# Optimization experiments

Measured on AMD Instinct MI355X. Metric: run time of the kernel, lower is better.

The kernel has to match this reference:

```python
import jax, jax.numpy as jnp
import numpy as np

B, T, C, HS = 4, 2048, 1024, 64

def setup_inputs() -> dict:
    key = jax.random.key(0)
    k1, k2, k3, k4 = jax.random.split(key, 4)
    x = jax.random.normal(k1, (B, T, C), dtype=jnp.float32)
    # torch Linear default init scale ~ 1/sqrt(fan_in); scale weights similarly
    s = C ** -0.5
    Wq = jax.random.normal(k2, (C, HS), dtype=jnp.float32) * s
    Wk = jax.random.normal(k3, (C, HS), dtype=jnp.float32) * s
    Wv = jax.random.normal(k4, (C, HS), dtype=jnp.float32) * s
    return {"x": x, "Wq": Wq, "Wk": Wk, "Wv": Wv}

def reference(x, Wq, Wk, Wv):
    B_, T_, C_ = x.shape
    q = x @ Wq          # [B,T,HS]
    k = x @ Wk          # [B,T,HS]
    v = x @ Wv          # [B,T,HS]
    scale = C_ ** -0.5  # note: module scales by input dim C, not head_size
    w = jnp.einsum('bqh,bkh->bqk', q, k) * scale  # [B,T,T]
    causal = jnp.tril(jnp.ones((T_, T_), dtype=bool))
    w = jnp.where(causal, w, -jnp.inf)
    a = jax.nn.softmax(w, axis=-1)  # dropout is identity (eval / drop_rate=0)
    return jnp.einsum('bqk,bkh->bqh', a, v)
```

## Files before the change

kernel.cpp:

```cpp
#include <hip/hip_runtime.h>
#include <math.h>

#define B_  4
#define T_  2048
#define C_  1024
#define HS_ 64
#define M_  (B_*T_)
#define NCAT 192
#define SCALE_ 0.03125f

typedef unsigned short ushort_t;
typedef short bf16x8 __attribute__((ext_vector_type(8)));
typedef float f32x4 __attribute__((ext_vector_type(4)));

static __device__ __forceinline__ unsigned short f2bf(float f) {
    union { float f; unsigned int u; } c; c.f = f;
    unsigned int u = c.u;
    return (unsigned short)((u + 0x7FFFu + ((u >> 16) & 1u)) >> 16);
}
static __device__ __forceinline__ unsigned short f2bf_fast(float f) {
    union { float f; unsigned int u; } c; c.f = f;
    return (unsigned short)((c.u + 0x8000u) >> 16);
}

__global__ void wconv_kernel(const float* __restrict__ Wq, const float* __restrict__ Wk,
                             const float* __restrict__ Wv, ushort_t* __restrict__ wt) {
    int idx = (blockIdx.x * 256 + threadIdx.x) * 4;
    int n = idx >> 10;
    int k0 = idx & 1023;
    const float* W = (n < 64) ? Wq : (n < 128) ? Wk : Wv;
    int nn = n & 63;
    ushort_t o0 = f2bf(W[(k0 + 0) * HS_ + nn]);
    ushort_t o1 = f2bf(W[(k0 + 1) * HS_ + nn]);
    ushort_t o2 = f2bf(W[(k0 + 2) * HS_ + nn]);
    ushort_t o3 = f2bf(W[(k0 + 3) * HS_ + nn]);
    uint2 d;
    d.x = (unsigned)o0 | ((unsigned)o1 << 16);
    d.y = (unsigned)o2 | ((unsigned)o3 << 16);
    *(uint2*)(wt + (size_t)n * C_ + k0) = d;
}

__global__ __launch_bounds__(512, 4) void proj_kernel(const float* __restrict__ x,
    const ushort_t* __restrict__ wt,
    ushort_t* __restrict__ qws, ushort_t* __restrict__ kws, ushort_t* __restrict__ vt) {
    __shared__ __align__(16) f32x4 red[4][12 * 64];

    int tid  = threadIdx.x;
    int wid  = tid >> 6;
    int lane = tid & 63;
    int qd   = lane >> 4;
    int lq   = lane & 15;
    int r0   = blockIdx.x * 16;

    f32x4 acc[12];
    #pragma unroll
    for (int i = 0; i < 12; i++) acc[i] = (f32x4){0.f,0.f,0.f,0.f};

    const float*    xp = x  + (size_t)(r0 + lq) * C_ + wid * 128 + qd * 8;
    const ushort_t* wp = wt + (size_t)lq * C_ + wid * 128 + qd * 8;

    #pragma unroll
    for (int i = 0; i < 4; i++) {
        float4 a0 = *(const float4*)(xp + i * 32);
        float4 a1 = *(const float4*)(xp + i * 32 + 4);
        union { bf16x8 v; ushort_t u[8]; } af;
        af.u[0] = f2bf(a0.x); af.u[1] = f2bf(a0.y); af.u[2] = f2bf(a0.z); af.u[3] = f2bf(a0.w);
        af.u[4] = f2bf(a1.x); af.u[5] = f2bf(a1.y); af.u[6] = f2bf(a1.z); af.u[7] = f2bf(a1.w);
        #pragma unroll
        for (int nt = 0; nt < 12; nt++) {
            bf16x8 bv = *(const bf16x8*)(wp + (size_t)nt * 16 * C_ + i * 32);
            acc[nt] = __builtin_amdgcn_mfma_f32_16x16x32_bf16(af.v, bv, acc[nt], 0, 0, 0);
        }
    }

    if (wid >= 4) {
        #pragma unroll
        for (int nt = 0; nt < 12; nt++) red[wid - 4][nt * 64 + lane] = acc[nt];
    }
    __syncthreads();
    if (wid < 4) {
        #pragma unroll
        for (int nt = 0; nt < 12; nt++) acc[nt] += red[wid][nt * 64 + lane];
    }
    __syncthreads();
    if (wid == 2 || wid == 3) {
        #pragma unroll
        for (int nt = 0; nt < 12; nt++) red[wid][nt * 64 + lane] = acc[nt];
    }
    __syncthreads();
    if (wid < 2) {
        #pragma unroll
        for (int nt = 0; nt < 12; nt++) acc[nt] += red[wid + 2][nt * 64 + lane];
    }
    __syncthreads();
    if (wid == 1) {
        #pragma unroll
        for (int nt = 0; nt < 12; nt++) red[0][nt * 64 + lane] = acc[nt];
    }
    __syncthreads();
    if (wid == 0) {
        #pragma unroll
        for (int nt = 0; nt < 12; nt++) {
            acc[nt] += red[0][nt * 64 + lane];
            int outn = nt >> 2;
            int col  = (nt & 3) * 16 + lq;
            #pragma unroll
            for (int r = 0; r < 4; r++) {
                int row = r0 + qd * 4 + r;
                float v = acc[nt][r];
                if (outn == 0) v *= SCALE_;
                ushort_t val = f2bf(v);
                if (outn == 0)      qws[(size_t)row * HS_ + col] = val;
                else if (outn == 1) kws[(size_t)row * HS_ + col] = val;
                else {
                    int b = row >> 11, t = row & 2047;
                    vt[((size_t)b * 64 + col) * T_ + t] = val;
                }
            }
        }
    }
}

__global__ __launch_bounds__(512, 2) void flash_kernel(const ushort_t* __restrict__ qws,
    const ushort_t* __restrict__ kws, const ushort_t* __restrict__ vt,
    float* __restrict__ out) {
    __shared__ __align__(16) unsigned char pool[18432];

    int tid  = threadIdx.x;
    int wid  = tid >> 6;
    int lane = tid & 63;
    int qd   = lane >> 4;
    int lq   = lane & 15;
    int ts   = wid >> 2;
    int ws   = wid & 3;

    int batch = blockIdx.y;
    int p     = blockIdx.x;
    int tile  = ts ? (127 - p) : p;
    int q0    = tile * 16;
    int qrow  = q0 + lq;
    int grow  = batch * T_ + qrow;
    int nU    = (tile + 4) >> 2;

    bf16x8 qf[2];
    #pragma unroll
    for (int st = 0; st < 2; st++)
        qf[st] = *(const bf16x8*)(qws + (size_t)grow * HS_ + st * 32 + qd * 8);

    float lsum = 0.f;
    f32x4 O[4];
    #pragma unroll
    for (int nt = 0; nt < 4; nt++) O[nt] = (f32x4){0.f,0.f,0.f,0.f};

    ushort_t* pw = (ushort_t*)pool + wid * 1152 + lq * 72;
    const ushort_t* kp    = kws + (size_t)batch * T_ * HS_;
    const ushort_t* vbase = vt  + (size_t)batch * 64 * T_;

    for (int u = ws; u < nU; u += 4) {
        int kb = u * 64;

        bf16x8 kf[8], vf[8];
        #pragma unroll
        for (int sub = 0; sub < 4; sub++)
            #pragma unroll
            for (int st = 0; st < 2; st++)
                kf[sub * 2 + st] = *(const bf16x8*)(kp + (size_t)(kb + sub * 16 + lq) * HS_ + st * 32 + qd * 8);
        #pragma unroll
        for (int nt = 0; nt < 4; nt++)
            #pragma unroll
            for (int kk = 0; kk < 2; kk++)
                vf[nt * 2 + kk] = *(const bf16x8*)(vbase + ((size_t)nt * 16 + lq) * T_ + kb + kk * 32 + qd * 8);

        f32x4 S[4];
        #pragma unroll
        for (int sub = 0; sub < 4; sub++) {
            f32x4 s = (f32x4){0.f,0.f,0.f,0.f};
            #pragma unroll
            for (int st = 0; st < 2; st++)
                s = __builtin_amdgcn_mfma_f32_16x16x32_bf16(kf[sub * 2 + st], qf[st], s, 0, 0, 0);
            S[sub] = s;
        }

        if (kb + 64 > q0) {
            #pragma unroll
            for (int sub = 0; sub < 4; sub++)
                #pragma unroll
                for (int r = 0; r < 4; r++) {
                    int key = kb + sub * 16 + qd * 4 + r;
                    float pv = (key <= qrow) ? __expf(S[sub][r]) : 0.f;
                    S[sub][r] = pv;
                    lsum += pv;
                }
        } else {
            #pragma unroll
            for (int sub = 0; sub < 4; sub++)
                #pragma unroll
                for (int r = 0; r < 4; r++) {
                    float pv = __expf(S[sub][r]);
                    S[sub][r] = pv;
                    lsum += pv;
                }
        }

        #pragma unroll
        for (int sub = 0; sub < 4; sub++) {
            uint2 d;
            d.x = (unsigned)f2bf_fast(S[sub][0]) | ((unsigned)f2bf_fast(S[sub][1]) << 16);
            d.y = (unsigned)f2bf_fast(S[sub][2]) | ((unsigned)f2bf_fast(S[sub][3]) << 16);
            *(uint2*)(pw + sub * 16 + qd * 4) = d;
        }
        bf16x8 pf0 = *(const bf16x8*)(pw + qd * 8);
        bf16x8 pf1 = *(const bf16x8*)(pw + 32 + qd * 8);

        #pragma unroll
        for (int nt = 0; nt < 4; nt++) {
            O[nt] = __builtin_amdgcn_mfma_f32_16x16x32_bf16(vf[nt * 2 + 0], pf0, O[nt], 0, 0, 0);
            O[nt] = __builtin_amdgcn_mfma_f32_16x16x32_bf16(vf[nt * 2 + 1], pf1, O[nt], 0, 0, 0);
        }
    }

    f32x4* red  = (f32x4*)pool;
    float* lred = (float*)(pool + 16384);
    __syncthreads();
    if (ws >= 2) {
        int sl = ts * 2 + (ws - 2);
        f32x4* rs = red + (size_t)sl * 256;
        #pragma unroll
        for (int nt = 0; nt < 4; nt++) rs[nt * 64 + lane] = O[nt];
        lred[sl * 64 + lane] = lsum;
    }
    __syncthreads();
    if (ws < 2) {
        int sl = ts * 2 + ws;
        f32x4* rs = red + (size_t)sl * 256;
        #pragma unroll
        for (int nt = 0; nt < 4; nt++) O[nt] += rs[nt * 64 + lane];
        lsum += lred[sl * 64 + lane];
    }
    __syncthreads();
    if (ws == 1) {
        int sl = ts * 2;
        f32x4* rs = red + (size_t)sl * 256;
        #pragma unroll
        for (int nt = 0; nt < 4; nt++) rs[nt * 64 + lane] = O[nt];
        lred[sl * 64 + lane] = lsum;
    }
    __syncthreads();
    if (ws == 0) {
        int sl = ts * 2;
        f32x4* rs = red + (size_t)sl * 256;
        #pragma unroll
        for (int nt = 0; nt < 4; nt++) O[nt] += rs[nt * 64 + lane];
        lsum += lred[sl * 64 + lane];
        lsum += __shfl_xor(lsum, 16, 64);
        lsum += __shfl_xor(lsum, 32, 64);
        float li = 1.f / lsum;
        #pragma unroll
        for (int nt = 0; nt < 4; nt++) {
            f32x4 o = O[nt] * li;
            *(f32x4*)(out + (size_t)grow * HS_ + nt * 16 + qd * 4) = o;
        }
    }
}

extern "C" void kernel_launch(void* const* d_in, const int* in_sizes, int n_in,
                              void* d_out, int out_size, void* d_ws, size_t ws_size,
                              hipStream_t stream) {
    const float* x  = (const float*)d_in[0];
    const float* Wq = (const float*)d_in[1];
    const float* Wk = (const float*)d_in[2];
    const float* Wv = (const float*)d_in[3];
    float* out = (float*)d_out;

    ushort_t* wt  = (ushort_t*)d_ws;
    ushort_t* qws = wt  + (size_t)NCAT * C_;
    ushort_t* kws = qws + (size_t)M_ * HS_;
    ushort_t* vt  = kws + (size_t)M_ * HS_;

    wconv_kernel<<<NCAT * C_ / (256 * 4), 256, 0, stream>>>(Wq, Wk, Wv, wt);
    proj_kernel<<<512, 512, 0, stream>>>(x, wt, qws, kws, vt);
    flash_kernel<<<dim3(64, 4), 512, 0, stream>>>(qws, kws, vt, out);
}
```

Baseline: 121.3 us.

## Restructure QKV projection into LDS-tiled GEMM with 2D warp tiling

The projection kernel used to split K across 8 warps, with each warp reading its own bf16 weights and fp32 x straight from global memory, then reduce across warps through shared memory. It now stages 32-row x tiles (converted to bf16) and the full 192-column weight slice into padded LDS per 128-wide K step, and assigns each warp a 16x48 output tile. This removes the cross-warp reduction and the redundant global weight loads, at the cost of two barriers per K step, fewer blocks (256) and a lower occupancy bound.

```diff
diff --git a/kernel.cpp b/kernel.cpp
--- a/kernel.cpp
+++ b/kernel.cpp
@@ -40,82 +40,85 @@
     *(uint2*)(wt + (size_t)n * C_ + k0) = d;
 }
 
-__global__ __launch_bounds__(512, 4) void proj_kernel(const float* __restrict__ x,
+__global__ __launch_bounds__(512, 2) void proj_kernel(const float* __restrict__ x,
     const ushort_t* __restrict__ wt,
     ushort_t* __restrict__ qws, ushort_t* __restrict__ kws, ushort_t* __restrict__ vt) {
-    __shared__ __align__(16) f32x4 red[4][12 * 64];
+    __shared__ __align__(16) ushort_t lds[32 * 136 + 192 * 136];
+    ushort_t* xs  = lds;
+    ushort_t* wsl = lds + 32 * 136;
 
     int tid  = threadIdx.x;
     int wid  = tid >> 6;
     int lane = tid & 63;
     int qd   = lane >> 4;
     int lq   = lane & 15;
-    int r0   = blockIdx.x * 16;
-
-    f32x4 acc[12];
-    #pragma unroll
-    for (int i = 0; i < 12; i++) acc[i] = (f32x4){0.f,0.f,0.f,0.f};
-
-    const float*    xp = x  + (size_t)(r0 + lq) * C_ + wid * 128 + qd * 8;
-    const ushort_t* wp = wt + (size_t)lq * C_ + wid * 128 + qd * 8;
-
-    #pragma unroll
-    for (int i = 0; i < 4; i++) {
-        float4 a0 = *(const float4*)(xp + i * 32);
-        float4 a1 = *(const float4*)(xp + i * 32 + 4);
-        union { bf16x8 v; ushort_t u[8]; } af;
-        af.u[0] = f2bf(a0.x); af.u[1] = f2bf(a0.y); af.u[2] = f2bf(a0.z); af.u[3] = f2bf(a0.w);
-        af.u[4] = f2bf(a1.x); af.u[5] = f2bf(a1.y); af.u[6] = f2bf(a1.z); af.u[7] = f2bf(a1.w);
-        #pragma unroll
-        for (int nt = 0; nt < 12; nt++) {
-            bf16x8 bv = *(const bf16x8*)(wp + (size_t)nt * 16 * C_ + i * 32);
-            acc[nt] = __builtin_amdgcn_mfma_f32_16x16x32_bf16(af.v, bv, acc[nt], 0, 0, 0);
-        }
-    }
-
-    if (wid >= 4) {
-        #pragma unroll
-        for (int nt = 0; nt < 12; nt++) red[wid - 4][nt * 64 + lane] = acc[nt];
-    }
-    __syncthreads();
-    if (wid < 4) {
-        #pragma unroll
-        for (int nt = 0; nt < 12; nt++) acc[nt] += red[wid][nt * 64 + lane];
-    }
-    __syncthreads();
-    if (wid == 2 || wid == 3) {
-        #pragma unroll
-        for (int nt = 0; nt < 12; nt++) red[wid][nt * 64 + lane] = acc[nt];
-    }
-    __syncthreads();
-    if (wid < 2) {
-        #pragma unroll
-        for (int nt = 0; nt < 12; nt++) acc[nt] += red[wid + 2][nt * 64 + lane];
-    }
-    __syncthreads();
-    if (wid == 1) {
-        #pragma unroll
-        for (int nt = 0; nt < 12; nt++) red[0][nt * 64 + lane] = acc[nt];
-    }
-    __syncthreads();
-    if (wid == 0) {
-        #pragma unroll
-        for (int nt = 0; nt < 12; nt++) {
-            acc[nt] += red[0][nt * 64 + lane];
-            int outn = nt >> 2;
-            int col  = (nt & 3) * 16 + lq;
-            #pragma unroll
-            for (int r = 0; r < 4; r++) {
-                int row = r0 + qd * 4 + r;
-                float v = acc[nt][r];
-                if (outn == 0) v *= SCALE_;
-                ushort_t val = f2bf(v);
-                if (outn == 0)      qws[(size_t)row * HS_ + col] = val;
-                else if (outn == 1) kws[(size_t)row * HS_ + col] = val;
-                else {
-                    int b = row >> 11, t = row & 2047;
-                    vt[((size_t)b * 64 + col) * T_ + t] = val;
-                }
+    int mi   = wid >> 2;
+    int nj   = wid & 3;
+    int r0   = blockIdx.x * 32;
+
+    f32x4 acc[3];
+    #pragma unroll
+    for (int i = 0; i < 3; i++) acc[i] = (f32x4){0.f,0.f,0.f,0.f};
+
+    int xrow0 = tid >> 5,  xc0 = (tid & 31);
+    int xrow1 = (tid + 512) >> 5, xc1 = ((tid + 512) & 31);
+
+    for (int ks = 0; ks < 8; ks++) {
+        float4 xv0 = *(const float4*)(x + (size_t)(r0 + xrow0) * C_ + ks * 128 + xc0 * 4);
+        float4 xv1 = *(const float4*)(x + (size_t)(r0 + xrow1) * C_ + ks * 128 + xc1 * 4);
+        uint4 wv[6];
+        #pragma unroll
+        for (int j = 0; j < 6; j++) {
+            int cid = tid + j * 512;
+            int n   = cid >> 4, c16 = cid & 15;
+            wv[j] = *(const uint4*)(wt + (size_t)n * C_ + ks * 128 + c16 * 8);
+        }
+        __syncthreads();
+        {
+            uint2 p0, p1;
+            p0.x = (unsigned)f2bf(xv0.x) | ((unsigned)f2bf(xv0.y) << 16);
+            p0.y = (unsigned)f2bf(xv0.z) | ((unsigned)f2bf(xv0.w) << 16);
+            p1.x = (unsigned)f2bf(xv1.x) | ((unsigned)f2bf(xv1.y) << 16);
+            p1.y = (unsigned)f2bf(xv1.z) | ((unsigned)f2bf(xv1.w) << 16);
+            *(uint2*)(xs + xrow0 * 136 + xc0 * 4) = p0;
+            *(uint2*)(xs + xrow1 * 136 + xc1 * 4) = p1;
+            #pragma unroll
+            for (int j = 0; j < 6; j++) {
+                int cid = tid + j * 512;
+                int n   = cid >> 4, c16 = cid & 15;
+                *(uint4*)(wsl + n * 136 + c16 * 8) = wv[j];
+            }
+        }
+        __syncthreads();
+
+        const ushort_t* xrow = xs + (mi * 16 + lq) * 136;
+        #pragma unroll
+        for (int i = 0; i < 4; i++) {
+            bf16x8 af = *(const bf16x8*)(xrow + qd * 8 + i * 32);
+            #pragma unroll
+            for (int nt = 0; nt < 3; nt++) {
+                bf16x8 bv = *(const bf16x8*)(wsl + (nj * 48 + nt * 16 + lq) * 136 + qd * 8 + i * 32);
+                acc[nt] = __builtin_amdgcn_mfma_f32_16x16x32_bf16(af, bv, acc[nt], 0, 0, 0);
+            }
+        }
+    }
+
+    #pragma unroll
+    for (int nt = 0; nt < 3; nt++) {
+        int n    = nj * 48 + nt * 16 + lq;
+        int outn = n >> 6;
+        int col  = n & 63;
+        #pragma unroll
+        for (int r = 0; r < 4; r++) {
+            int row = r0 + mi * 16 + qd * 4 + r;
+            float v = acc[nt][r];
+            if (outn == 0) v *= SCALE_;
+            ushort_t val = f2bf(v);
+            if (outn == 0)      qws[(size_t)row * HS_ + col] = val;
+            else if (outn == 1) kws[(size_t)row * HS_ + col] = val;
+            else {
+                int b = row >> 11, t = row & 2047;
+                vt[((size_t)b * 64 + col) * T_ + t] = val;
             }
         }
     }
@@ -278,6 +281,6 @@
     ushort_t* vt  = kws + (size_t)M_ * HS_;
 
     wconv_kernel<<<NCAT * C_ / (256 * 4), 256, 0, stream>>>(Wq, Wk, Wv, wt);
-    proj_kernel<<<512, 512, 0, stream>>>(x, wt, qws, kws, vt);
+    proj_kernel<<<256, 512, 0, stream>>>(x, wt, qws, kws, vt);
     flash_kernel<<<dim3(64, 4), 512, 0, stream>>>(qws, kws, vt, out);
 }
```

New measurement: 134.2 us. +10.6%, slower.

## Pre-pack weights in MFMA fragment order and stage bf16 x tile in LDS

Applied to the files above, without the earlier changes.

The weight conversion kernel now writes bf16 weights already laid out in per-lane MFMA fragment order, so each lane in the projection kernel reads one contiguous 16-byte chunk instead of strided rows. The projection kernel loads its 16-row x tile with coalesced float4 reads, converts it to bf16 once into padded shared memory, and then feeds MFMA from LDS. The shared pool is reused for the cross-wave reduction, which adds an extra barrier and needs 48KB of LDS per block, and that may limit occupancy.

```diff
diff --git a/kernel.cpp b/kernel.cpp
--- a/kernel.cpp
+++ b/kernel.cpp
@@ -8,6 +8,7 @@
 #define M_  (B_*T_)
 #define NCAT 192
 #define SCALE_ 0.03125f
+#define XPAD 1032
 
 typedef unsigned short ushort_t;
 typedef short bf16x8 __attribute__((ext_vector_type(8)));
@@ -24,26 +25,25 @@
 }
 
 __global__ void wconv_kernel(const float* __restrict__ Wq, const float* __restrict__ Wk,
-                             const float* __restrict__ Wv, ushort_t* __restrict__ wt) {
-    int idx = (blockIdx.x * 256 + threadIdx.x) * 4;
-    int n = idx >> 10;
-    int k0 = idx & 1023;
-    const float* W = (n < 64) ? Wq : (n < 128) ? Wk : Wv;
-    int nn = n & 63;
-    ushort_t o0 = f2bf(W[(k0 + 0) * HS_ + nn]);
-    ushort_t o1 = f2bf(W[(k0 + 1) * HS_ + nn]);
-    ushort_t o2 = f2bf(W[(k0 + 2) * HS_ + nn]);
-    ushort_t o3 = f2bf(W[(k0 + 3) * HS_ + nn]);
-    uint2 d;
-    d.x = (unsigned)o0 | ((unsigned)o1 << 16);
-    d.y = (unsigned)o2 | ((unsigned)o3 << 16);
-    *(uint2*)(wt + (size_t)n * C_ + k0) = d;
+                             const float* __restrict__ Wv, ushort_t* __restrict__ wtp) {
+    int l = threadIdx.x & 63;
+    int g = blockIdx.x * 4 + (threadIdx.x >> 6);
+    int c  = g / 12;
+    int nt = g % 12;
+    const float* W = (nt < 4) ? Wq : (nt < 8) ? Wk : Wv;
+    int nn = (nt & 3) * 16 + (l & 15);
+    int k0 = c * 32 + (l >> 4) * 8;
+    union { bf16x8 v; ushort_t u[8]; } pk;
+    #pragma unroll
+    for (int e = 0; e < 8; e++)
+        pk.u[e] = f2bf(W[(size_t)(k0 + e) * HS_ + nn]);
+    *(bf16x8*)(wtp + ((size_t)g * 64 + l) * 8) = pk.v;
 }
 
 __global__ __launch_bounds__(512, 4) void proj_kernel(const float* __restrict__ x,
-    const ushort_t* __restrict__ wt,
+    const ushort_t* __restrict__ wtp,
     ushort_t* __restrict__ qws, ushort_t* __restrict__ kws, ushort_t* __restrict__ vt) {
-    __shared__ __align__(16) f32x4 red[4][12 * 64];
+    __shared__ __align__(16) unsigned char pool[49152];
 
     int tid  = threadIdx.x;
     int wid  = tid >> 6;
@@ -52,27 +52,47 @@
     int lq   = lane & 15;
     int r0   = blockIdx.x * 16;
 
+    ushort_t* xs = (ushort_t*)pool;
+    {
+        float4 xv[8];
+        #pragma unroll
+        for (int j = 0; j < 8; j++) {
+            int flat4 = j * 512 + tid;
+            int row   = flat4 >> 8;
+            int c4    = flat4 & 255;
+            xv[j] = *(const float4*)(x + (size_t)(r0 + row) * C_ + c4 * 4);
+        }
+        #pragma unroll
+        for (int j = 0; j < 8; j++) {
+            int flat4 = j * 512 + tid;
+            int row   = flat4 >> 8;
+            int c4    = flat4 & 255;
+            uint2 p;
+            p.x = (unsigned)f2bf(xv[j].x) | ((unsigned)f2bf(xv[j].y) << 16);
+            p.y = (unsigned)f2bf(xv[j].z) | ((unsigned)f2bf(xv[j].w) << 16);
+            *(uint2*)(xs + row * XPAD + c4 * 4) = p;
+        }
+    }
+    __syncthreads();
+
     f32x4 acc[12];
     #pragma unroll
     for (int i = 0; i < 12; i++) acc[i] = (f32x4){0.f,0.f,0.f,0.f};
 
-    const float*    xp = x  + (size_t)(r0 + lq) * C_ + wid * 128 + qd * 8;
-    const ushort_t* wp = wt + (size_t)lq * C_ + wid * 128 + qd * 8;
-
+    const ushort_t* xrow = xs + lq * XPAD + wid * 128 + qd * 8;
     #pragma unroll
     for (int i = 0; i < 4; i++) {
-        float4 a0 = *(const float4*)(xp + i * 32);
-        float4 a1 = *(const float4*)(xp + i * 32 + 4);
-        union { bf16x8 v; ushort_t u[8]; } af;
-        af.u[0] = f2bf(a0.x); af.u[1] = f2bf(a0.y); af.u[2] = f2bf(a0.z); af.u[3] = f2bf(a0.w);
-        af.u[4] = f2bf(a1.x); af.u[5] = f2bf(a1.y); af.u[6] = f2bf(a1.z); af.u[7] = f2bf(a1.w);
+        bf16x8 af = *(const bf16x8*)(xrow + i * 32);
         #pragma unroll
         for (int nt = 0; nt < 12; nt++) {
-            bf16x8 bv = *(const bf16x8*)(wp + (size_t)nt * 16 * C_ + i * 32);
-            acc[nt] = __builtin_amdgcn_mfma_f32_16x16x32_bf16(af.v, bv, acc[nt], 0, 0, 0);
-        }
-    }
-
+            bf16x8 bv = *(const bf16x8*)(wtp +
+                (((size_t)(wid * 4 + i) * 12 + nt) * 64 + lane) * 8);
+            acc[nt] = __builtin_amdgcn_mfma_f32_16x16x32_bf16(af, bv, acc[nt], 0, 0, 0);
+        }
+    }
+
+    __syncthreads();
+    f32x4 (*red)[12 * 64] = (f32x4 (*)[12 * 64])pool;
     if (wid >= 4) {
         #pragma unroll
         for (int nt = 0; nt < 12; nt++) red[wid - 4][nt * 64 + lane] = acc[nt];
@@ -272,12 +292,12 @@
     const float* Wv = (const float*)d_in[3];
     float* out = (float*)d_out;
 
-    ushort_t* wt  = (ushort_t*)d_ws;
-    ushort_t* qws = wt  + (size_t)NCAT * C_;
+    ushort_t* wtp = (ushort_t*)d_ws;
+    ushort_t* qws = wtp + (size_t)384 * 64 * 8;
     ushort_t* kws = qws + (size_t)M_ * HS_;
     ushort_t* vt  = kws + (size_t)M_ * HS_;
 
-    wconv_kernel<<<NCAT * C_ / (256 * 4), 256, 0, stream>>>(Wq, Wk, Wv, wt);
-    proj_kernel<<<512, 512, 0, stream>>>(x, wt, qws, kws, vt);
+    wconv_kernel<<<96, 256, 0, stream>>>(Wq, Wk, Wv, wtp);
+    proj_kernel<<<512, 512, 0, stream>>>(x, wtp, qws, kws, vt);
     flash_kernel<<<dim3(64, 4), 512, 0, stream>>>(qws, kws, vt, out);
 }
```

After: 106.8 us (median of 2 runs). 1.14x faster.
